# Kernel optimization log

Hardware: AMD Instinct MI355X
Metric: run time of the kernel (lower is better)

Reference implementation:

```python
import jax, jax.numpy as jnp
import numpy as np

NUM_HEADS = 16

def setup_inputs() -> dict:
    key = jax.random.key(0)
    ks = jax.random.split(key, 8)
    B, S, D = 2, 2048, 1024
    w = lambda k: jax.random.normal(k, (D, D), dtype=jnp.float32) * 0.02
    return {
        "x": jax.random.normal(ks[0], (B, S, D), dtype=jnp.float32),
        "attn_mask": jnp.zeros((S, S), dtype=jnp.float32),
        "key_padding_mask": jnp.zeros((B, S), dtype=bool),
        "Wq": w(ks[1]), "bq": jnp.zeros((D,), jnp.float32),
        "Wk": w(ks[2]), "bk": jnp.zeros((D,), jnp.float32),
        "Wv": w(ks[3]), "bv": jnp.zeros((D,), jnp.float32),
        "Wg": w(ks[4]), "bg": jnp.full((D,), 0.5, jnp.float32),  # gate_bias_init=0.5
        "Wo": w(ks[5]), "bo": jnp.zeros((D,), jnp.float32),
    }

def reference(x, attn_mask, key_padding_mask, Wq, bq, Wk, bk, Wv, bv, Wg, bg, Wo, bo):
    B, S, D = x.shape
    H = NUM_HEADS
    hd = D // H
    scale = jnp.sqrt(jnp.float32(hd)).astype(x.dtype)

    def split_heads(t):  # (B,S,D) -> (B,H,S,hd)
        return t.reshape(B, S, H, hd).transpose(0, 2, 1, 3)

    q = split_heads(x @ Wq + bq)
    k = split_heads(x @ Wk + bk)
    v = split_heads(x @ Wv + bv)

    scores = jnp.einsum("bhqd,bhkd->bhqk", q, k) / scale
    scores = scores + attn_mask[None, None, :, :]
    scores = jnp.where(key_padding_mask[:, None, None, :], -jnp.inf, scores)

    attn_weights = jax.nn.softmax(scores, axis=-1)          # (B,H,S,S)
    attn_out = jnp.einsum("bhqk,bhkd->bhqd", attn_weights, v)

    gate = jax.nn.sigmoid(x @ Wg + bg)                      # (B,S,D)
    gate = split_heads(gate)                                # (B,H,S,hd)
    attn_out = attn_out * gate

    attn_out = attn_out.transpose(0, 2, 1, 3).reshape(B, S, D)
    output = attn_out @ Wo + bo
    avg_attn = attn_weights.mean(axis=1)                    # (B,S,S)
    return output, avg_attn
```

## Files before the change

kernel.cpp:

```cpp
#include <hip/hip_runtime.h>
#include <hip/hip_bf16.h>

#define LOG2E 1.4426950408889634f

typedef short short8 __attribute__((ext_vector_type(8)));
typedef float floatx4 __attribute__((ext_vector_type(4)));

__device__ __forceinline__ floatx4 mfma16(short8 a, short8 b, floatx4 c) {
    return __builtin_amdgcn_mfma_f32_16x16x32_bf16(a, b, c, 0, 0, 0);
}

__device__ __forceinline__ float fexp2(float x) { return __builtin_amdgcn_exp2f(x); }

__device__ __forceinline__ short f2bf(float f) {
    unsigned u = __builtin_bit_cast(unsigned, f);
    u += 0x7FFFu + ((u >> 16) & 1u);
    return (short)(u >> 16);
}
__device__ __forceinline__ unsigned bfpair(float a, float b) {
    unsigned ua = __builtin_bit_cast(unsigned, a);
    unsigned ub = __builtin_bit_cast(unsigned, b);
    ua += 0x7FFFu + ((ua >> 16) & 1u);
    ub += 0x7FFFu + ((ub >> 16) & 1u);
    return (ua >> 16) | (ub & 0xFFFF0000u);
}
__device__ __forceinline__ float bf2f(short s) {
    unsigned u = ((unsigned)(unsigned short)s) << 16;
    return __builtin_bit_cast(float, u);
}

__device__ __forceinline__ void glds16(const void* g, void* l) {
    __builtin_amdgcn_global_load_lds(
        (const __attribute__((address_space(1))) void*)g,
        (__attribute__((address_space(3))) void*)l, 16, 0, 0);
}

__device__ __forceinline__ short8 cvt8(const float* __restrict__ p) {
    float4 a = *reinterpret_cast<const float4*>(p);
    float4 b = *reinterpret_cast<const float4*>(p + 4);
    short8 r;
    r[0] = f2bf(a.x); r[1] = f2bf(a.y); r[2] = f2bf(a.z); r[3] = f2bf(a.w);
    r[4] = f2bf(b.x); r[5] = f2bf(b.y); r[6] = f2bf(b.z); r[7] = f2bf(b.w);
    return r;
}

__global__ __launch_bounds__(256) void cvt_x_kernel(
    const float* __restrict__ in, short* __restrict__ out, int n8)
{
    int i = blockIdx.x * blockDim.x + threadIdx.x;
    if (i < n8)
        *reinterpret_cast<short8*>(out + (size_t)i * 8) = cvt8(in + (size_t)i * 8);
}

__global__ __launch_bounds__(256) void cvt_wt_kernel(
    const float* __restrict__ W0, const float* __restrict__ W1,
    const float* __restrict__ W2, const float* __restrict__ W3,
    const float* __restrict__ W4, short* __restrict__ Wt)
{
    __shared__ short T[64 * 66];
    const int w = blockIdx.z;
    const float* W = (w == 0) ? W0 : (w == 1) ? W1 : (w == 2) ? W2 : (w == 3) ? W3 : W4;
    short* dst = Wt + (size_t)w * 1024 * 1024;
    const int kb = blockIdx.y * 64, nb = blockIdx.x * 64;
    const int t = threadIdx.x;
    const int r = t >> 2, c4 = (t & 3) * 16;
    *reinterpret_cast<short8*>(T + r * 66 + c4)     = cvt8(W + (size_t)(kb + r) * 1024 + nb + c4);
    *reinterpret_cast<short8*>(T + r * 66 + c4 + 8) = cvt8(W + (size_t)(kb + r) * 1024 + nb + c4 + 8);
    __syncthreads();
    short8 o0, o1;
    #pragma unroll
    for (int j = 0; j < 8; ++j) o0[j] = T[(c4 + j) * 66 + r];
    #pragma unroll
    for (int j = 0; j < 8; ++j) o1[j] = T[(c4 + 8 + j) * 66 + r];
    *reinterpret_cast<short8*>(dst + (size_t)(nb + r) * 1024 + kb + c4)     = o0;
    *reinterpret_cast<short8*>(dst + (size_t)(nb + r) * 1024 + kb + c4 + 8) = o1;
}

__global__ __launch_bounds__(256) void mask_prep(
    const float* __restrict__ amask, const unsigned char* __restrict__ kpm,
    float* __restrict__ Mc)
{
    const int b = blockIdx.z, q = blockIdx.y;
    const int p0 = threadIdx.x * 8;
    float o[8];
    #pragma unroll
    for (int i = 0; i < 8; ++i) {
        int p = p0 + i;
        int j = (p & ~31) | ((p >> 1) & 15) | ((p & 1) << 4);
        float kp = kpm[b * 2048 + j] ? -1.0e30f : 0.f;
        o[i] = amask[(size_t)q * 2048 + j] * LOG2E + kp;
    }
    float* dst = Mc + ((size_t)b * 2048 + q) * 2048 + p0;
    *reinterpret_cast<float4*>(dst)     = make_float4(o[0], o[1], o[2], o[3]);
    *reinterpret_cast<float4*>(dst + 4) = make_float4(o[4], o[5], o[6], o[7]);
}

__device__ __forceinline__ void gemm_core(
    const short* __restrict__ A, const short* __restrict__ Wt,
    int mbase, int nbase, short* Asm, short* Bsm, floatx4 (&acc)[4][4])
{
    const int tid = threadIdx.x;
    const int lane = tid & 63, wid = tid >> 6;
    const int L15 = lane & 15, g = lane >> 4;
    const int wm = (wid >> 1) * 64, wn = (wid & 1) * 64;

    const int rowoff = lane >> 3;
    const int choff = ((lane & 7) ^ rowoff) * 8;
    const short* aP = A  + (size_t)(mbase + wid * 32 + rowoff) * 1024 + choff;
    const short* bP = Wt + (size_t)(nbase + wid * 32 + rowoff) * 1024 + choff;
    short* aL = Asm + wid * 2048;
    short* bL = Bsm + wid * 2048;

    const int xb = L15 & 7;
    const int s0 = (g ^ xb) * 8;
    const int s1 = ((g ^ 4) ^ xb) * 8;

    for (int kb = 0; kb < 1024; kb += 64) {
        __syncthreads();
        #pragma unroll
        for (int j = 0; j < 4; ++j) glds16(aP + kb + j * 8192, aL + j * 512);
        #pragma unroll
        for (int j = 0; j < 4; ++j) glds16(bP + kb + j * 8192, bL + j * 512);
        __syncthreads();
        #pragma unroll
        for (int ks = 0; ks < 2; ++ks) {
            const int so = ks ? s1 : s0;
            short8 af[4], bf[4];
            #pragma unroll
            for (int mt = 0; mt < 4; ++mt)
                af[mt] = *reinterpret_cast<const short8*>(Asm + (wm + mt * 16 + L15) * 64 + so);
            #pragma unroll
            for (int nt = 0; nt < 4; ++nt)
                bf[nt] = *reinterpret_cast<const short8*>(Bsm + (wn + nt * 16 + L15) * 64 + so);
            #pragma unroll
            for (int mt = 0; mt < 4; ++mt)
                #pragma unroll
                for (int nt = 0; nt < 4; ++nt)
                    acc[mt][nt] = mfma16(af[mt], bf[nt], acc[mt][nt]);
        }
    }
}

__global__ __launch_bounds__(256) void qkvg_gemm(
    const short* __restrict__ A, const short* __restrict__ Wt5,
    const float* __restrict__ b0, const float* __restrict__ b1,
    const float* __restrict__ b2, const float* __restrict__ b3,
    short* __restrict__ dQ, short* __restrict__ dK,
    short* __restrict__ dV, short* __restrict__ dG)
{
    __shared__ short Asm[128 * 64];
    __shared__ short Bsm[128 * 64];
    const int z = blockIdx.z;
    const int mbase = blockIdx.y * 128, nbase = blockIdx.x * 128;
    floatx4 acc[4][4] = {};
    gemm_core(A, Wt5 + (size_t)z * 1048576, mbase, nbase, Asm, Bsm, acc);

    const int lane = threadIdx.x & 63, wid = threadIdx.x >> 6;
    const int L15 = lane & 15, g = lane >> 4;
    const int wm = (wid >> 1) * 64, wn = (wid & 1) * 64;
    const float* bz = (z == 0) ? b0 : (z == 1) ? b1 : (z == 2) ? b2 : b3;
    short* dst = (z == 0) ? dQ : (z == 1) ? dK : (z == 2) ? dV : dG;

    #pragma unroll
    for (int nt = 0; nt < 4; ++nt) {
        int col = nbase + wn + nt * 16 + L15;
        float bv = bz[col];
        #pragma unroll
        for (int mt = 0; mt < 4; ++mt) {
            #pragma unroll
            for (int r = 0; r < 4; ++r) {
                int row = mbase + wm + mt * 16 + g * 4 + r;
                float val = acc[mt][nt][r] + bv;
                int bb = row >> 11, s = row & 2047;
                int hh = col >> 6, dh = col & 63;
                if (z <= 1) {
                    dst[(((size_t)bb * 16 + hh) * 2048 + s) * 64 + dh] = f2bf(val);
                } else if (z == 2) {
                    int sp = (s & ~31) | ((s & 15) << 1) | ((s >> 4) & 1);
                    dst[(((size_t)bb * 16 + hh) * 64 + dh) * 2048 + sp] = f2bf(val);
                } else {
                    float e = fexp2(-val * LOG2E);
                    dst[(size_t)row * 1024 + col] = f2bf(__builtin_amdgcn_rcpf(1.0f + e));
                }
            }
        }
    }
}

__global__ __launch_bounds__(256) void out_gemm(
    const short* __restrict__ A, const short* __restrict__ Wt,
    const float* __restrict__ bias, float* __restrict__ out)
{
    __shared__ short Asm[128 * 64];
    __shared__ short Bsm[128 * 64];
    const int mbase = blockIdx.y * 128, nbase = blockIdx.x * 128;
    floatx4 acc[4][4] = {};
    gemm_core(A, Wt, mbase, nbase, Asm, Bsm, acc);

    const int lane = threadIdx.x & 63, wid = threadIdx.x >> 6;
    const int L15 = lane & 15, g = lane >> 4;
    const int wm = (wid >> 1) * 64, wn = (wid & 1) * 64;
    #pragma unroll
    for (int nt = 0; nt < 4; ++nt) {
        int col = nbase + wn + nt * 16 + L15;
        float bv = bias[col];
        #pragma unroll
        for (int mt = 0; mt < 4; ++mt)
            #pragma unroll
            for (int r = 0; r < 4; ++r) {
                int row = mbase + wm + mt * 16 + g * 4 + r;
                out[(size_t)row * 1024 + col] = acc[mt][nt][r] + bv;
            }
    }
}

__global__ __launch_bounds__(256) void flash_attn(
    const short* __restrict__ Q, const short* __restrict__ K,
    const short* __restrict__ Vt, const short* __restrict__ G,
    const float* __restrict__ Mc,
    short* __restrict__ att, float* __restrict__ inv_l)
{
    __shared__ short Ksm[2][32 * 64];
    __shared__ short Vsm[2][32 * 64];
    __shared__ short Psm[4][16 * 40];

    const int tid = threadIdx.x;
    const int lane = tid & 63, wid = tid >> 6;
    const int L15 = lane & 15, g = lane >> 4;
    const int b = blockIdx.z, h = blockIdx.x;
    const int bh = b * 16 + h;
    const int qb = blockIdx.y * 64 + wid * 16;
    const float SC = 0.125f * LOG2E;

    short8 aq0 = *reinterpret_cast<const short8*>(Q + ((size_t)bh * 2048 + qb + L15) * 64 + g * 8);
    short8 aq1 = *reinterpret_cast<const short8*>(Q + ((size_t)bh * 2048 + qb + L15) * 64 + 32 + g * 8);

    floatx4 O[4] = {};
    float l_r[4] = {0.f, 0.f, 0.f, 0.f};

    const int krow = lane >> 3;
    const int kch  = ((lane & 7) ^ krow) * 8;
    const short* kP = K + ((size_t)bh * 2048 + wid * 8 + krow) * 64 + kch;
    const int vsc  = (lane & 7) ^ krow;
    const int vhd  = wid * 16 + 2 * krow + (vsc >> 2);
    const short* vP = Vt + ((size_t)bh * 64 + vhd) * 2048 + (vsc & 3) * 8;
    short* kL[2] = { &Ksm[0][wid * 512], &Ksm[1][wid * 512] };
    short* vL[2] = { &Vsm[0][wid * 512], &Vsm[1][wid * 512] };

    const int x7 = L15 & 7;
    const int sk0 = (g ^ x7) * 8, sk1 = ((g ^ 4) ^ x7) * 8;
    const int sv = (((L15 & 1) * 4 + g) ^ ((L15 >> 1) & 7)) * 8;
    const int vp = (L15 >> 1) * 64;

    const float* mcP[4];
    #pragma unroll
    for (int r = 0; r < 4; ++r)
        mcP[r] = Mc + ((size_t)b * 2048 + qb + g * 4 + r) * 2048 + 2 * L15;

    glds16(kP, kL[0]);
    glds16(vP, vL[0]);
    float2 mc[4];
    #pragma unroll
    for (int r = 0; r < 4; ++r) mc[r] = *reinterpret_cast<const float2*>(mcP[r]);

    for (int kb = 0; kb < 2048; kb += 32) {
        const int cur = (kb >> 5) & 1;
        __syncthreads();
        const int nb = kb + 32;
        const bool more = nb < 2048;
        float2 nmc[4];
        if (more) {
            glds16(kP + (size_t)nb * 64, kL[cur ^ 1]);
            glds16(vP + nb, vL[cur ^ 1]);
            #pragma unroll
            for (int r = 0; r < 4; ++r) nmc[r] = *reinterpret_cast<const float2*>(mcP[r] + nb);
        }

        const short* Kb = Ksm[cur];
        const short* Vb = Vsm[cur];
        floatx4 s0 = {}, s1 = {};
        s0 = mfma16(aq0, *reinterpret_cast<const short8*>(Kb + L15 * 64 + sk0), s0);
        s0 = mfma16(aq1, *reinterpret_cast<const short8*>(Kb + L15 * 64 + sk1), s0);
        s1 = mfma16(aq0, *reinterpret_cast<const short8*>(Kb + (16 + L15) * 64 + sk0), s1);
        s1 = mfma16(aq1, *reinterpret_cast<const short8*>(Kb + (16 + L15) * 64 + sk1), s1);

        #pragma unroll
        for (int r = 0; r < 4; ++r) {
            float e0 = fexp2(s0[r] * SC + mc[r].x);
            float e1 = fexp2(s1[r] * SC + mc[r].y);
            l_r[r] += e0 + e1;
            *reinterpret_cast<unsigned*>(&Psm[wid][(g * 4 + r) * 40 + 2 * L15]) = bfpair(e0, e1);
        }
        short8 ap = *reinterpret_cast<const short8*>(&Psm[wid][L15 * 40 + g * 8]);
        #pragma unroll
        for (int t = 0; t < 4; ++t)
            O[t] = mfma16(ap, *reinterpret_cast<const short8*>(Vb + t * 512 + vp + sv), O[t]);

        if (more) {
            #pragma unroll
            for (int r = 0; r < 4; ++r) mc[r] = nmc[r];
        }
    }

    float inv[4];
    #pragma unroll
    for (int r = 0; r < 4; ++r) {
        float ls = l_r[r];
        ls += __shfl_xor(ls, 1);
        ls += __shfl_xor(ls, 2);
        ls += __shfl_xor(ls, 4);
        ls += __shfl_xor(ls, 8);
        inv[r] = 1.0f / ls;
        if (L15 == 0) inv_l[(size_t)bh * 2048 + qb + g * 4 + r] = inv[r];
    }
    #pragma unroll
    for (int t = 0; t < 4; ++t) {
        int col = h * 64 + t * 16 + L15;
        #pragma unroll
        for (int r = 0; r < 4; ++r) {
            size_t qr = qb + g * 4 + r;
            float gt = bf2f(G[((size_t)b * 2048 + qr) * 1024 + col]);
            att[((size_t)b * 2048 + qr) * 1024 + col] = f2bf(O[t][r] * inv[r] * gt);
        }
    }
}

__global__ __launch_bounds__(256) void avg_attn_kernel(
    const short* __restrict__ Q, const short* __restrict__ K,
    const float* __restrict__ inv_l, float* mca)
{
    __shared__ short Ksm[2][128 * 64];
    const int tid = threadIdx.x;
    const int lane = tid & 63, wid = tid >> 6;
    const int L15 = lane & 15, g = lane >> 4;
    const int b = blockIdx.z;
    const int qb = blockIdx.y * 64 + wid * 16;
    const int ks = blockIdx.x * 128;
    const float SC = 0.125f * LOG2E;

    float pm[4][2][4];
    #pragma unroll
    for (int c = 0; c < 4; ++c)
        #pragma unroll
        for (int r = 0; r < 4; ++r) {
            size_t qr = qb + g * 4 + r;
            float2 m = *reinterpret_cast<const float2*>(
                mca + ((size_t)b * 2048 + qr) * 2048 + ks + c * 32 + 2 * L15);
            pm[c][0][r] = m.x;
            pm[c][1][r] = m.y;
        }
    float av[4][2][4] = {};

    const int rowoff = lane >> 3;
    const int choff = ((lane & 7) ^ rowoff) * 8;
    const int x7 = L15 & 7;
    const int sk0 = (g ^ x7) * 8, sk1 = ((g ^ 4) ^ x7) * 8;
    short* kL[2] = { &Ksm[0][wid * 2048], &Ksm[1][wid * 2048] };

    {
        const short* p = K + ((size_t)(b * 16) * 2048 + ks + wid * 32 + rowoff) * 64 + choff;
        #pragma unroll
        for (int j = 0; j < 4; ++j) glds16(p + j * 512, kL[0] + j * 512);
    }
    short8 aq0 = *reinterpret_cast<const short8*>(Q + ((size_t)(b * 16) * 2048 + qb + L15) * 64 + g * 8);
    short8 aq1 = *reinterpret_cast<const short8*>(Q + ((size_t)(b * 16) * 2048 + qb + L15) * 64 + 32 + g * 8);
    float iv[4];
    #pragma unroll
    for (int r = 0; r < 4; ++r) iv[r] = inv_l[(size_t)(b * 16) * 2048 + qb + g * 4 + r];

    for (int h = 0; h < 16; ++h) {
        __syncthreads();
        short8 naq0, naq1;
        float niv[4];
        if (h < 15) {
            int nbh = b * 16 + h + 1;
            const short* p = K + ((size_t)nbh * 2048 + ks + wid * 32 + rowoff) * 64 + choff;
            #pragma unroll
            for (int j = 0; j < 4; ++j) glds16(p + j * 512, kL[(h + 1) & 1] + j * 512);
            naq0 = *reinterpret_cast<const short8*>(Q + ((size_t)nbh * 2048 + qb + L15) * 64 + g * 8);
            naq1 = *reinterpret_cast<const short8*>(Q + ((size_t)nbh * 2048 + qb + L15) * 64 + 32 + g * 8);
            #pragma unroll
            for (int r = 0; r < 4; ++r) niv[r] = inv_l[(size_t)nbh * 2048 + qb + g * 4 + r];
        }

        const short* Kb = Ksm[h & 1];
        #pragma unroll
        for (int c = 0; c < 4; ++c) {
            const short* kbase = Kb + c * 32 * 64;
            floatx4 s0 = {}, s1 = {};
            s0 = mfma16(aq0, *reinterpret_cast<const short8*>(kbase + L15 * 64 + sk0), s0);
            s0 = mfma16(aq1, *reinterpret_cast<const short8*>(kbase + L15 * 64 + sk1), s0);
            s1 = mfma16(aq0, *reinterpret_cast<const short8*>(kbase + (16 + L15) * 64 + sk0), s1);
            s1 = mfma16(aq1, *reinterpret_cast<const short8*>(kbase + (16 + L15) * 64 + sk1), s1);
            #pragma unroll
            for (int r = 0; r < 4; ++r) {
                av[c][0][r] += fexp2(s0[r] * SC + pm[c][0][r]) * iv[r];
                av[c][1][r] += fexp2(s1[r] * SC + pm[c][1][r]) * iv[r];
            }
        }
        if (h < 15) {
            aq0 = naq0; aq1 = naq1;
            #pragma unroll
            for (int r = 0; r < 4; ++r) iv[r] = niv[r];
        }
    }
    #pragma unroll
    for (int c = 0; c < 4; ++c)
        #pragma unroll
        for (int t = 0; t < 2; ++t)
            #pragma unroll
            for (int r = 0; r < 4; ++r) {
                size_t qr = qb + g * 4 + r;
                int col = ks + c * 32 + t * 16 + L15;
                mca[((size_t)b * 2048 + qr) * 2048 + col] = av[c][t][r] * 0.0625f;
            }
}

extern "C" void kernel_launch(void* const* d_in, const int* in_sizes, int n_in,
                              void* d_out, int out_size, void* d_ws, size_t ws_size,
                              hipStream_t stream)
{
    const float* x  = (const float*)d_in[0];
    const float* amask = (const float*)d_in[1];
    const unsigned char* kpm = (const unsigned char*)d_in[2];
    const float* Wq = (const float*)d_in[3];
    const float* bq = (const float*)d_in[4];
    const float* Wk = (const float*)d_in[5];
    const float* bk = (const float*)d_in[6];
    const float* Wv = (const float*)d_in[7];
    const float* bv = (const float*)d_in[8];
    const float* Wg = (const float*)d_in[9];
    const float* bg = (const float*)d_in[10];
    const float* Wo = (const float*)d_in[11];
    const float* bo = (const float*)d_in[12];

    char* ws = (char*)d_ws;
    const size_t MB = 1u << 20;
    short* Xb    = (short*)(ws);
    short* Att   = Xb;
    short* Qw    = (short*)(ws + 8 * MB);
    short* Kw    = (short*)(ws + 16 * MB);
    short* Vt    = (short*)(ws + 24 * MB);
    short* Gw    = (short*)(ws + 32 * MB);
    short* Wt    = (short*)(ws + 40 * MB);
    float* stats = (float*)(ws + 50 * MB);

    float* outp = (float*)d_out;
    float* avgp = (float*)d_out + 4194304;

    cvt_x_kernel<<<2048, 256, 0, stream>>>(x, Xb, 524288);
    cvt_wt_kernel<<<dim3(16, 16, 5), 256, 0, stream>>>(Wq, Wk, Wv, Wg, Wo, Wt);
    mask_prep<<<dim3(1, 2048, 2), 256, 0, stream>>>(amask, kpm, avgp);

    qkvg_gemm<<<dim3(8, 32, 4), 256, 0, stream>>>(Xb, Wt, bq, bk, bv, bg, Qw, Kw, Vt, Gw);

    flash_attn<<<dim3(16, 32, 2), 256, 0, stream>>>(Qw, Kw, Vt, Gw, avgp, Att, stats);

    avg_attn_kernel<<<dim3(16, 32, 2), 256, 0, stream>>>(Qw, Kw, stats, avgp);

    out_gemm<<<dim3(8, 32), 256, 0, stream>>>(Att, Wt + 4 * 1048576, bo, outp);
}
```

Before: 329.2 us.

## Skip mask loads when masks are all zero; widen flash tiles to 64 keys and 8 waves

mask_prep now sets a device flag via ballot and atomicOr if any attention-mask or padding entry is nonzero. flash_attn and avg_attn branch on this flag and skip reading the precomputed mask when it is clear. flash_attn is also restructured to 512 threads (8 waves, 128 queries per block) with 64-key tiles, and K and V loading is split between wave groups. The mask check is exact rather than input-specific, but it adds a memset and an atomic, and the new tiling raises LDS use and register pressure.

New measurement: 296.0 us. 10.1% less time.

```diff
diff --git a/kernel.cpp b/kernel.cpp
--- a/kernel.cpp
+++ b/kernel.cpp
@@ -78,21 +78,25 @@
 
 __global__ __launch_bounds__(256) void mask_prep(
     const float* __restrict__ amask, const unsigned char* __restrict__ kpm,
-    float* __restrict__ Mc)
+    float* __restrict__ Mc, int* __restrict__ flag)
 {
     const int b = blockIdx.z, q = blockIdx.y;
     const int p0 = threadIdx.x * 8;
     float o[8];
+    bool nz = false;
     #pragma unroll
     for (int i = 0; i < 8; ++i) {
         int p = p0 + i;
         int j = (p & ~31) | ((p >> 1) & 15) | ((p & 1) << 4);
-        float kp = kpm[b * 2048 + j] ? -1.0e30f : 0.f;
-        o[i] = amask[(size_t)q * 2048 + j] * LOG2E + kp;
+        unsigned char kb = kpm[b * 2048 + j];
+        float a = amask[(size_t)q * 2048 + j];
+        nz |= (a != 0.f) || (kb != 0);
+        o[i] = a * LOG2E + (kb ? -1.0e30f : 0.f);
     }
     float* dst = Mc + ((size_t)b * 2048 + q) * 2048 + p0;
     *reinterpret_cast<float4*>(dst)     = make_float4(o[0], o[1], o[2], o[3]);
     *reinterpret_cast<float4*>(dst + 4) = make_float4(o[4], o[5], o[6], o[7]);
+    if (__ballot(nz) && ((threadIdx.x & 63) == 0)) atomicOr(flag, 1);
 }
 
 __device__ __forceinline__ void gemm_core(
@@ -214,22 +218,20 @@
     }
 }
 
-__global__ __launch_bounds__(256) void flash_attn(
+template<bool MASKED>
+__device__ __forceinline__ void flash_body(
     const short* __restrict__ Q, const short* __restrict__ K,
     const short* __restrict__ Vt, const short* __restrict__ G,
-    const float* __restrict__ Mc,
-    short* __restrict__ att, float* __restrict__ inv_l)
-{
-    __shared__ short Ksm[2][32 * 64];
-    __shared__ short Vsm[2][32 * 64];
-    __shared__ short Psm[4][16 * 40];
-
+    const float* __restrict__ Mc, short* __restrict__ att,
+    float* __restrict__ inv_l,
+    short* Ksm, short* Vsm, short* Psm)
+{
     const int tid = threadIdx.x;
     const int lane = tid & 63, wid = tid >> 6;
     const int L15 = lane & 15, g = lane >> 4;
     const int b = blockIdx.z, h = blockIdx.x;
     const int bh = b * 16 + h;
-    const int qb = blockIdx.y * 64 + wid * 16;
+    const int qb = blockIdx.y * 128 + wid * 16;
     const float SC = 0.125f * LOG2E;
 
     short8 aq0 = *reinterpret_cast<const short8*>(Q + ((size_t)bh * 2048 + qb + L15) * 64 + g * 8);
@@ -240,65 +242,98 @@
 
     const int krow = lane >> 3;
     const int kch  = ((lane & 7) ^ krow) * 8;
-    const short* kP = K + ((size_t)bh * 2048 + wid * 8 + krow) * 64 + kch;
-    const int vsc  = (lane & 7) ^ krow;
-    const int vhd  = wid * 16 + 2 * krow + (vsc >> 2);
-    const short* vP = Vt + ((size_t)bh * 64 + vhd) * 2048 + (vsc & 3) * 8;
-    short* kL[2] = { &Ksm[0][wid * 512], &Ksm[1][wid * 512] };
-    short* vL[2] = { &Vsm[0][wid * 512], &Vsm[1][wid * 512] };
+    const bool isK = wid < 4;
+    const int sw = isK ? wid : (wid - 4);
+    const short* gP;
+    if (isK) {
+        gP = K + ((size_t)bh * 2048 + sw * 16 + krow) * 64 + kch;
+    } else {
+        const int vsc = (lane & 7) ^ krow;
+        const int vhd = sw * 16 + 2 * krow + (vsc >> 2);
+        gP = Vt + ((size_t)bh * 64 + vhd) * 2048 + (vsc & 3) * 8;
+    }
 
     const int x7 = L15 & 7;
     const int sk0 = (g ^ x7) * 8, sk1 = ((g ^ 4) ^ x7) * 8;
     const int sv = (((L15 & 1) * 4 + g) ^ ((L15 >> 1) & 7)) * 8;
     const int vp = (L15 >> 1) * 64;
 
+    short* Pw = Psm + wid * 1152;
+
     const float* mcP[4];
-    #pragma unroll
-    for (int r = 0; r < 4; ++r)
-        mcP[r] = Mc + ((size_t)b * 2048 + qb + g * 4 + r) * 2048 + 2 * L15;
-
-    glds16(kP, kL[0]);
-    glds16(vP, vL[0]);
-    float2 mc[4];
-    #pragma unroll
-    for (int r = 0; r < 4; ++r) mc[r] = *reinterpret_cast<const float2*>(mcP[r]);
-
-    for (int kb = 0; kb < 2048; kb += 32) {
-        const int cur = (kb >> 5) & 1;
+    float2 mc0[4], mc1[4];
+    if (MASKED) {
+        #pragma unroll
+        for (int r = 0; r < 4; ++r) {
+            mcP[r] = Mc + ((size_t)b * 2048 + qb + g * 4 + r) * 2048 + 2 * L15;
+            mc0[r] = *reinterpret_cast<const float2*>(mcP[r]);
+            mc1[r] = *reinterpret_cast<const float2*>(mcP[r] + 32);
+        }
+    }
+
+    if (isK) {
+        glds16(gP,       Ksm + sw * 1024);
+        glds16(gP + 512, Ksm + sw * 1024 + 512);
+    } else {
+        glds16(gP,      Vsm + sw * 512);
+        glds16(gP + 32, Vsm + 2048 + sw * 512);
+    }
+
+    for (int kb = 0; kb < 2048; kb += 64) {
+        const int cur = (kb >> 6) & 1;
         __syncthreads();
-        const int nb = kb + 32;
+        const int nb = kb + 64;
         const bool more = nb < 2048;
-        float2 nmc[4];
+        float2 nmc0[4], nmc1[4];
         if (more) {
-            glds16(kP + (size_t)nb * 64, kL[cur ^ 1]);
-            glds16(vP + nb, vL[cur ^ 1]);
-            #pragma unroll
-            for (int r = 0; r < 4; ++r) nmc[r] = *reinterpret_cast<const float2*>(mcP[r] + nb);
-        }
-
-        const short* Kb = Ksm[cur];
-        const short* Vb = Vsm[cur];
-        floatx4 s0 = {}, s1 = {};
-        s0 = mfma16(aq0, *reinterpret_cast<const short8*>(Kb + L15 * 64 + sk0), s0);
-        s0 = mfma16(aq1, *reinterpret_cast<const short8*>(Kb + L15 * 64 + sk1), s0);
-        s1 = mfma16(aq0, *reinterpret_cast<const short8*>(Kb + (16 + L15) * 64 + sk0), s1);
-        s1 = mfma16(aq1, *reinterpret_cast<const short8*>(Kb + (16 + L15) * 64 + sk1), s1);
+            if (isK) {
+                glds16(gP + (size_t)nb * 64,       Ksm + (cur ^ 1) * 4096 + sw * 1024);
+                glds16(gP + (size_t)nb * 64 + 512, Ksm + (cur ^ 1) * 4096 + sw * 1024 + 512);
+            } else {
+                glds16(gP + nb,      Vsm + (cur ^ 1) * 4096 + sw * 512);
+                glds16(gP + nb + 32, Vsm + (cur ^ 1) * 4096 + 2048 + sw * 512);
+            }
+            if (MASKED) {
+                #pragma unroll
+                for (int r = 0; r < 4; ++r) {
+                    nmc0[r] = *reinterpret_cast<const float2*>(mcP[r] + nb);
+                    nmc1[r] = *reinterpret_cast<const float2*>(mcP[r] + nb + 32);
+                }
+            }
+        }
+
+        const short* Kb = Ksm + cur * 4096;
+        floatx4 s[4];
+        #pragma unroll
+        for (int kt = 0; kt < 4; ++kt) {
+            s[kt] = {};
+            s[kt] = mfma16(aq0, *reinterpret_cast<const short8*>(Kb + (kt * 16 + L15) * 64 + sk0), s[kt]);
+            s[kt] = mfma16(aq1, *reinterpret_cast<const short8*>(Kb + (kt * 16 + L15) * 64 + sk1), s[kt]);
+        }
 
         #pragma unroll
         for (int r = 0; r < 4; ++r) {
-            float e0 = fexp2(s0[r] * SC + mc[r].x);
-            float e1 = fexp2(s1[r] * SC + mc[r].y);
-            l_r[r] += e0 + e1;
-            *reinterpret_cast<unsigned*>(&Psm[wid][(g * 4 + r) * 40 + 2 * L15]) = bfpair(e0, e1);
-        }
-        short8 ap = *reinterpret_cast<const short8*>(&Psm[wid][L15 * 40 + g * 8]);
-        #pragma unroll
-        for (int t = 0; t < 4; ++t)
-            O[t] = mfma16(ap, *reinterpret_cast<const short8*>(Vb + t * 512 + vp + sv), O[t]);
-
-        if (more) {
-            #pragma unroll
-            for (int r = 0; r < 4; ++r) mc[r] = nmc[r];
+            float e0 = fexp2(s[0][r] * SC + (MASKED ? mc0[r].x : 0.f));
+            float e1 = fexp2(s[1][r] * SC + (MASKED ? mc0[r].y : 0.f));
+            float e2 = fexp2(s[2][r] * SC + (MASKED ? mc1[r].x : 0.f));
+            float e3 = fexp2(s[3][r] * SC + (MASKED ? mc1[r].y : 0.f));
+            l_r[r] += (e0 + e1) + (e2 + e3);
+            *reinterpret_cast<unsigned*>(&Pw[(g * 4 + r) * 72 + 2 * L15])      = bfpair(e0, e1);
+            *reinterpret_cast<unsigned*>(&Pw[(g * 4 + r) * 72 + 32 + 2 * L15]) = bfpair(e2, e3);
+        }
+        short8 ap0 = *reinterpret_cast<const short8*>(&Pw[L15 * 72 + g * 8]);
+        short8 ap1 = *reinterpret_cast<const short8*>(&Pw[L15 * 72 + 32 + g * 8]);
+        const short* Vb0 = Vsm + cur * 4096;
+        const short* Vb1 = Vb0 + 2048;
+        #pragma unroll
+        for (int t = 0; t < 4; ++t) {
+            O[t] = mfma16(ap0, *reinterpret_cast<const short8*>(Vb0 + t * 512 + vp + sv), O[t]);
+            O[t] = mfma16(ap1, *reinterpret_cast<const short8*>(Vb1 + t * 512 + vp + sv), O[t]);
+        }
+
+        if (MASKED && more) {
+            #pragma unroll
+            for (int r = 0; r < 4; ++r) { mc0[r] = nmc0[r]; mc1[r] = nmc1[r]; }
         }
     }
 
@@ -325,9 +360,24 @@
     }
 }
 
+__global__ __launch_bounds__(512, 4) void flash_attn(
+    const short* __restrict__ Q, const short* __restrict__ K,
+    const short* __restrict__ Vt, const short* __restrict__ G,
+    const float* __restrict__ Mc, const int* __restrict__ flag,
+    short* __restrict__ att, float* __restrict__ inv_l)
+{
+    __shared__ short Ksm[2 * 4096];
+    __shared__ short Vsm[2 * 4096];
+    __shared__ short Psm[8 * 1152];
+    if (*flag)
+        flash_body<true>(Q, K, Vt, G, Mc, att, inv_l, Ksm, Vsm, Psm);
+    else
+        flash_body<false>(Q, K, Vt, G, Mc, att, inv_l, Ksm, Vsm, Psm);
+}
+
 __global__ __launch_bounds__(256) void avg_attn_kernel(
     const short* __restrict__ Q, const short* __restrict__ K,
-    const float* __restrict__ inv_l, float* mca)
+    const float* __restrict__ inv_l, float* mca, const int* __restrict__ flag)
 {
     __shared__ short Ksm[2][128 * 64];
     const int tid = threadIdx.x;
@@ -339,16 +389,26 @@
     const float SC = 0.125f * LOG2E;
 
     float pm[4][2][4];
-    #pragma unroll
-    for (int c = 0; c < 4; ++c)
-        #pragma unroll
-        for (int r = 0; r < 4; ++r) {
-            size_t qr = qb + g * 4 + r;
-            float2 m = *reinterpret_cast<const float2*>(
-                mca + ((size_t)b * 2048 + qr) * 2048 + ks + c * 32 + 2 * L15);
-            pm[c][0][r] = m.x;
-            pm[c][1][r] = m.y;
-        }
+    if (*flag) {
+        #pragma unroll
+        for (int c = 0; c < 4; ++c)
+            #pragma unroll
+            for (int r = 0; r < 4; ++r) {
+                size_t qr = qb + g * 4 + r;
+                float2 m = *reinterpret_cast<const float2*>(
+                    mca + ((size_t)b * 2048 + qr) * 2048 + ks + c * 32 + 2 * L15);
+                pm[c][0][r] = m.x;
+                pm[c][1][r] = m.y;
+            }
+    } else {
+        #pragma unroll
+        for (int c = 0; c < 4; ++c)
+            #pragma unroll
+            for (int r = 0; r < 4; ++r) {
+                pm[c][0][r] = 0.f;
+                pm[c][1][r] = 0.f;
+            }
+    }
     float av[4][2][4] = {};
 
     const int rowoff = lane >> 3;
@@ -444,19 +504,22 @@
     short* Gw    = (short*)(ws + 32 * MB);
     short* Wt    = (short*)(ws + 40 * MB);
     float* stats = (float*)(ws + 50 * MB);
+    int*   flagp = (int*)(ws + 50 * MB + 262144);
 
     float* outp = (float*)d_out;
     float* avgp = (float*)d_out + 4194304;
 
+    hipMemsetAsync(flagp, 0, sizeof(int), stream);
+
     cvt_x_kernel<<<2048, 256, 0, stream>>>(x, Xb, 524288);
     cvt_wt_kernel<<<dim3(16, 16, 5), 256, 0, stream>>>(Wq, Wk, Wv, Wg, Wo, Wt);
-    mask_prep<<<dim3(1, 2048, 2), 256, 0, stream>>>(amask, kpm, avgp);
+    mask_prep<<<dim3(1, 2048, 2), 256, 0, stream>>>(amask, kpm, avgp, flagp);
 
     qkvg_gemm<<<dim3(8, 32, 4), 256, 0, stream>>>(Xb, Wt, bq, bk, bv, bg, Qw, Kw, Vt, Gw);
 
-    flash_attn<<<dim3(16, 32, 2), 256, 0, stream>>>(Qw, Kw, Vt, Gw, avgp, Att, stats);
-
-    avg_attn_kernel<<<dim3(16, 32, 2), 256, 0, stream>>>(Qw, Kw, stats, avgp);
+    flash_attn<<<dim3(16, 16, 2), 512, 0, stream>>>(Qw, Kw, Vt, Gw, avgp, flagp, Att, stats);
+
+    avg_attn_kernel<<<dim3(16, 32, 2), 256, 0, stream>>>(Qw, Kw, stats, avgp, flagp);
 
     out_gemm<<<dim3(8, 32), 256, 0, stream>>>(Att, Wt + 4 * 1048576, bo, outp);
 }
```
